# Kernel tuning notes

Hardware: AMD Instinct MI355X
Metric: run time of the kernel (lower is better)

## Reference

```python
import jax, jax.numpy as jnp
import numpy as np


def setup_inputs() -> dict:
    key = jax.random.key(0)
    ks = jax.random.split(key, 8)
    B, D, H1, H2, C = 262144, 256, 256, 128, 8
    s1 = 1.0 / np.sqrt(D)
    s2 = 1.0 / np.sqrt(H1)
    s3 = 1.0 / np.sqrt(H2)
    return {
        "x": jax.random.normal(ks[0], (B, D), dtype=jnp.float32),
        "W1": jax.random.normal(ks[1], (D, H1), dtype=jnp.float32) * s1,
        "b1": jnp.zeros((H1,), dtype=jnp.float32),
        "W2": jax.random.normal(ks[2], (H1, H2), dtype=jnp.float32) * s2,
        "b2": jnp.zeros((H2,), dtype=jnp.float32),
        "W3": jax.random.normal(ks[3], (H2, C), dtype=jnp.float32) * s3,
        "b3": jnp.zeros((C,), dtype=jnp.float32),
        "weibull_alpha": jnp.ones((C,), dtype=jnp.float32) * 2.0,
        "weibull_beta": jax.random.uniform(ks[4], (C,), dtype=jnp.float32, minval=0.5, maxval=2.0),
        "weibull_tau": jnp.zeros((C,), dtype=jnp.float32),
        "activation_vectors": jax.random.normal(ks[5], (C, H2), dtype=jnp.float32),
    }


def reference(x, W1, b1, W2, b2, W3, b3, weibull_alpha, weibull_beta, weibull_tau, activation_vectors):
    # MLP trunk (eval mode: dropout = identity)
    h = jax.nn.relu(x @ W1 + b1)          # [B, 256]
    act = jax.nn.relu(h @ W2 + b2)        # [B, H]
    logits = act @ W3 + b3                # [B, C]

    # per-class Euclidean distances via ||a-v||^2 = ||a||^2 - 2 a.v + ||v||^2
    a2 = jnp.sum(act * act, axis=1, keepdims=True)                 # [B, 1]
    v2 = jnp.sum(activation_vectors * activation_vectors, axis=1)  # [C]
    d2 = a2 - 2.0 * (act @ activation_vectors.T) + v2[None, :]     # [B, C]
    distances = jnp.sqrt(jnp.maximum(d2, 0.0))

    # Weibull CDF calibration, max over classes
    safe_beta = jnp.maximum(weibull_beta, 1e-6)                    # [C]
    safe_x = jnp.maximum(distances - weibull_tau[None, :], 0.0)    # [B, C]
    cdf = 1.0 - jnp.exp(-jnp.power(safe_x / safe_beta[None, :], weibull_alpha[None, :]))
    unknown_probs = jnp.max(cdf, axis=1)                           # [B]

    # conditional rescale of logits where unknown prob > 0.5
    scale = jnp.where(unknown_probs > 0.5, 1.0 - unknown_probs, 1.0)
    return logits * scale[:, None]
```

## Files before the change

kernel.cpp:

```cpp
#include <hip/hip_runtime.h>
#include <hip/hip_bf16.h>
#include <math.h>

typedef __attribute__((ext_vector_type(16))) float f32x16;

#define MFMA8(A, B, C) __builtin_amdgcn_mfma_f32_32x32x16_fp8_fp8((long)(A), (long)(B), (C), 0, 0, 0)

__device__ __forceinline__ int pk4(float a, float b, float c, float d) {
    int w = __builtin_amdgcn_cvt_pk_fp8_f32(a, b, 0, false);
    w = __builtin_amdgcn_cvt_pk_fp8_f32(c, d, w, true);
    return w;
}


__global__ void prep_pack(const float* __restrict__ W1, const float* __restrict__ W2,
                          const float* __restrict__ W3, const float* __restrict__ AV,
                          char* __restrict__ wp) {
    int j = blockIdx.x * 256 + threadIdx.x;
    float f[8];
    if (j < 8192) {
        int kc = j >> 8, m = j & 255;
        #pragma unroll
        for (int i = 0; i < 8; ++i) f[i] = W1[(kc * 8 + i) * 256 + m] * 16.f;
        int2 t; t.x = pk4(f[0], f[1], f[2], f[3]); t.y = pk4(f[4], f[5], f[6], f[7]);
        *(int2*)(wp + (size_t)j * 8) = t;
    } else if (j < 12288) {
        int jj = j - 8192; int kc = jj >> 7, m = jj & 127;
        #pragma unroll
        for (int i = 0; i < 8; ++i) f[i] = W2[(kc * 8 + i) * 128 + m] * 16.f;
        int2 t; t.x = pk4(f[0], f[1], f[2], f[3]); t.y = pk4(f[4], f[5], f[6], f[7]);
        *(int2*)(wp + 65536 + (size_t)jj * 8) = t;
    } else if (j < 12800) {
        int jj = j - 12288; int kc = jj >> 5, m = jj & 31;
        #pragma unroll
        for (int i = 0; i < 8; ++i) {
            int k = kc * 8 + i;
            float v = 0.f;
            if (m < 8)       v = W3[k * 8 + m] * 8.f;
            else if (m < 16) v = AV[(m - 8) * 128 + k];
            f[i] = v;
        }
        int2 t; t.x = pk4(f[0], f[1], f[2], f[3]); t.y = pk4(f[4], f[5], f[6], f[7]);
        *(int2*)(wp + 98304 + (size_t)jj * 8) = t;
    }
}

__global__ void prep_small(const float* __restrict__ AV, const float* __restrict__ b1,
                           const float* __restrict__ b2, float* __restrict__ v2,
                           float* __restrict__ b1p, float* __restrict__ b2p) {
    int t = threadIdx.x;
    {
        int mt = t >> 5, g = (t >> 4) & 1, r = t & 15;
        b1p[t] = b1[mt * 32 + 4 * g + (r & 3) + 8 * (r >> 2)];
    }
    if (t < 128) {
        int mt = t >> 5, g = (t >> 4) & 1, r = t & 15;
        b2p[t] = b2[mt * 32 + 4 * g + (r & 3) + 8 * (r >> 2)];
    }
    if (t < 64) {
        int c = t >> 3, jj = t & 7;
        float s = 0.f;
        for (int k = jj * 16; k < jj * 16 + 16; ++k) { float a = AV[c * 128 + k]; s = fmaf(a, a, s); }
        s += __shfl_xor(s, 1); s += __shfl_xor(s, 2); s += __shfl_xor(s, 4);
        if (jj == 0) v2[c] = s;
    }
}

#define LDS_H 16384

__global__ __launch_bounds__(256, 4)
void openmax_mfma(const float* __restrict__ x,
                  const float* __restrict__ b3,
                  const float* __restrict__ walpha, const float* __restrict__ wbeta,
                  const float* __restrict__ wtau,
                  const char* __restrict__ wpack, const float* __restrict__ v2g,
                  const float* __restrict__ b1p, const float* __restrict__ b2p,
                  float* __restrict__ out) {
    __shared__ __align__(16) char smem[32768];
    const int tid = threadIdx.x;
    const int l = tid & 63, wv = tid >> 6;
    const int lo = l & 31, g = l >> 5;
    const long row0 = (long)blockIdx.x * 64;

    const unsigned long long* Ap1 = (const unsigned long long*)wpack;
    const unsigned long long* Ap2 = (const unsigned long long*)(wpack + 65536);
    const unsigned long long* Ap3 = (const unsigned long long*)(wpack + 98304);

    const float4* xg = (const float4*)(x + row0 * 256);
    float4 xv[16];
    #pragma unroll
    for (int i = 0; i < 16; ++i) xv[i] = xg[i * 256 + tid];

    const int aRow1 = wv * 64 + lo;
    unsigned long long pa0[2], pa1[2];
    #pragma unroll
    for (int p = 0; p < 2; ++p) {
        int kc = p * 2 + g;
        pa0[p] = Ap1[kc * 256 + aRow1];
        pa1[p] = Ap1[kc * 256 + aRow1 + 32];
    }

    #pragma unroll
    for (int i = 0; i < 16; ++i) {
        int fc = i * 256 + tid;
        int row = fc >> 6, c4 = fc & 63;
        int hc = c4 >> 1, half = c4 & 1;
        int w = pk4(xv[i].x, xv[i].y, xv[i].z, xv[i].w);
        *(int*)(smem + row * 256 + (((hc ^ (row & 31)) << 3) + half * 4)) = w;
    }
    __syncthreads();

    {
        unsigned long long pb0[2], pb1[2];
        #pragma unroll
        for (int p = 0; p < 2; ++p) {
            int kc = p * 2 + g;
            pb0[p] = *(const unsigned long long*)(smem + lo * 256 + ((kc ^ lo) << 3));
            pb1[p] = *(const unsigned long long*)(smem + (32 + lo) * 256 + ((kc ^ lo) << 3));
        }
        f32x16 a00, a01, a10, a11;
        #pragma unroll
        for (int i = 0; i < 16; ++i) { a00[i] = 0.f; a01[i] = 0.f; a10[i] = 0.f; a11[i] = 0.f; }
        #pragma unroll
        for (int ks = 0; ks < 16; ++ks) {
            const int slot = ks & 1;
            unsigned long long A0 = pa0[slot], A1 = pa1[slot], B0 = pb0[slot], B1 = pb1[slot];
            if (ks < 14) {
                int kc = (ks + 2) * 2 + g;
                pa0[slot] = Ap1[kc * 256 + aRow1];
                pa1[slot] = Ap1[kc * 256 + aRow1 + 32];
                pb0[slot] = *(const unsigned long long*)(smem + lo * 256 + ((kc ^ lo) << 3));
                pb1[slot] = *(const unsigned long long*)(smem + (32 + lo) * 256 + ((kc ^ lo) << 3));
            }
            a00 = MFMA8(A0, B0, a00);
            a01 = MFMA8(A0, B1, a01);
            a10 = MFMA8(A1, B0, a10);
            a11 = MFMA8(A1, B1, a11);
        }
        #pragma unroll
        for (int mt = 0; mt < 2; ++mt) {
            const float* bp = b1p + ((wv * 2 + mt) * 2 + g) * 16;
            float bia[16];
            *(float4*)(bia)      = *(const float4*)(bp);
            *(float4*)(bia + 4)  = *(const float4*)(bp + 4);
            *(float4*)(bia + 8)  = *(const float4*)(bp + 8);
            *(float4*)(bia + 12) = *(const float4*)(bp + 12);
            #pragma unroll
            for (int nt = 0; nt < 2; ++nt) {
                const f32x16& A = (mt == 0) ? (nt == 0 ? a00 : a01)
                                            : (nt == 0 ? a10 : a11);
                int b = nt * 32 + lo;
                int base = LDS_H + b * 256 + g * 4;
                #pragma unroll
                for (int q = 0; q < 4; ++q) {
                    float v0 = fmaxf(fmaf(A[4 * q + 0], 0.0625f, bia[4 * q + 0]), 0.f);
                    float v1 = fmaxf(fmaf(A[4 * q + 1], 0.0625f, bia[4 * q + 1]), 0.f);
                    float v2_ = fmaxf(fmaf(A[4 * q + 2], 0.0625f, bia[4 * q + 2]), 0.f);
                    float v3 = fmaxf(fmaf(A[4 * q + 3], 0.0625f, bia[4 * q + 3]), 0.f);
                    int hc = (wv * 2 + mt) * 4 + q;
                    *(int*)(smem + base + ((hc ^ (b & 31)) << 3)) = pk4(v0, v1, v2_, v3);
                }
            }
        }
    }

    const int aRow2 = wv * 32 + lo;
    unsigned long long pa2[2];
    #pragma unroll
    for (int p = 0; p < 2; ++p) {
        int kc = p * 2 + g;
        pa2[p] = Ap2[kc * 128 + aRow2];
    }
    __syncthreads();

    {
        unsigned long long pb0[2], pb1[2];
        #pragma unroll
        for (int p = 0; p < 2; ++p) {
            int kc = p * 2 + g;
            pb0[p] = *(const unsigned long long*)(smem + LDS_H + lo * 256 + ((kc ^ lo) << 3));
            pb1[p] = *(const unsigned long long*)(smem + LDS_H + (32 + lo) * 256 + ((kc ^ lo) << 3));
        }
        f32x16 c0, c1;
        #pragma unroll
        for (int i = 0; i < 16; ++i) { c0[i] = 0.f; c1[i] = 0.f; }
        #pragma unroll
        for (int ks = 0; ks < 16; ++ks) {
            const int slot = ks & 1;
            unsigned long long A = pa2[slot], B0 = pb0[slot], B1 = pb1[slot];
            if (ks < 14) {
                int kc = (ks + 2) * 2 + g;
                pa2[slot] = Ap2[kc * 128 + aRow2];
                pb0[slot] = *(const unsigned long long*)(smem + LDS_H + lo * 256 + ((kc ^ lo) << 3));
                pb1[slot] = *(const unsigned long long*)(smem + LDS_H + (32 + lo) * 256 + ((kc ^ lo) << 3));
            }
            c0 = MFMA8(A, B0, c0);
            c1 = MFMA8(A, B1, c1);
        }
        const float* bp = b2p + (wv * 2 + g) * 16;
        float bia[16];
        *(float4*)(bia)      = *(const float4*)(bp);
        *(float4*)(bia + 4)  = *(const float4*)(bp + 4);
        *(float4*)(bia + 8)  = *(const float4*)(bp + 8);
        *(float4*)(bia + 12) = *(const float4*)(bp + 12);
        #pragma unroll
        for (int nt = 0; nt < 2; ++nt) {
            const f32x16& A = (nt == 0) ? c0 : c1;
            int b = nt * 32 + lo;
            int base = b * 128 + g * 4;
            float ss = 0.f;
            #pragma unroll
            for (int q = 0; q < 4; ++q) {
                float v0 = fmaxf(fmaf(A[4 * q + 0], 0.0625f, bia[4 * q + 0]), 0.f);
                float v1 = fmaxf(fmaf(A[4 * q + 1], 0.0625f, bia[4 * q + 1]), 0.f);
                float v2_ = fmaxf(fmaf(A[4 * q + 2], 0.0625f, bia[4 * q + 2]), 0.f);
                float v3 = fmaxf(fmaf(A[4 * q + 3], 0.0625f, bia[4 * q + 3]), 0.f);
                ss += v0 * v0 + v1 * v1 + v2_ * v2_ + v3 * v3;
                int ac = wv * 4 + q;
                *(int*)(smem + base + ((ac ^ (b & 15)) << 3)) = pk4(v0, v1, v2_, v3);
            }
            ss += __shfl_xor(ss, 32);
            if (g == 0) *(float*)(smem + 8192 + (wv * 64 + b) * 4) = ss;
        }
    }

    unsigned long long pa3[8];
    float4 e_b3[2], e_v2[2], e_al[2], e_be[2], e_ta[2];
    if (wv < 2) {
        #pragma unroll
        for (int p = 0; p < 8; ++p) {
            int kc = p * 2 + g;
            pa3[p] = Ap3[kc * 32 + lo];
        }
        e_b3[0] = *(const float4*)(b3);     e_b3[1] = *(const float4*)(b3 + 4);
        e_v2[0] = *(const float4*)(v2g);    e_v2[1] = *(const float4*)(v2g + 4);
        e_al[0] = *(const float4*)(walpha); e_al[1] = *(const float4*)(walpha + 4);
        e_be[0] = *(const float4*)(wbeta);  e_be[1] = *(const float4*)(wbeta + 4);
        e_ta[0] = *(const float4*)(wtau);   e_ta[1] = *(const float4*)(wtau + 4);
    }
    __syncthreads();

    if (wv < 2) {
        const int b = wv * 32 + lo;
        unsigned long long pb[8];
        #pragma unroll
        for (int p = 0; p < 8; ++p) {
            int kc = p * 2 + g;
            pb[p] = *(const unsigned long long*)(smem + b * 128 + ((kc ^ (b & 15)) << 3));
        }
        f32x16 acc;
        #pragma unroll
        for (int i = 0; i < 16; ++i) acc[i] = 0.f;
        #pragma unroll
        for (int ks = 0; ks < 8; ++ks)
            acc = MFMA8(pa3[ks], pb[ks], acc);

        float oth[8];
        #pragma unroll
        for (int j = 0; j < 8; ++j) oth[j] = __shfl_xor(acc[j], 32);

        float a2v = 0.f;
        #pragma unroll
        for (int wq = 0; wq < 4; ++wq)
            a2v += *(const float*)(smem + 8192 + (wq * 64 + b) * 4);

        float m = 0.f, outv[8];
        #pragma unroll
        for (int c = 0; c < 8; ++c) {
            float lgv = ((c >> 2) == g) ? acc[c & 3]       : oth[c & 3];
            float dtv = ((c >> 2) == g) ? acc[4 + (c & 3)] : oth[4 + (c & 3)];
            float v2c = e_v2[c >> 2][c & 3];
            float d2 = a2v - 2.f * dtv + v2c;
            float dist = sqrtf(fmaxf(d2, 0.f));
            float sb = fmaxf(e_be[c >> 2][c & 3], 1e-6f);
            float sx = fmaxf(dist - e_ta[c >> 2][c & 3], 0.f);
            float t = sx / sb;
            float y = exp2f(e_al[c >> 2][c & 3] * log2f(t));
            float cdf = 1.f - expf(-y);
            m = fmaxf(m, cdf);
            outv[c] = fmaf(lgv, 0.125f, e_b3[c >> 2][c & 3]);
        }
        float scale = (m > 0.5f) ? (1.f - m) : 1.f;
        if (g == 0) {
            float4 o0 = { outv[0] * scale, outv[1] * scale, outv[2] * scale, outv[3] * scale };
            float4 o1 = { outv[4] * scale, outv[5] * scale, outv[6] * scale, outv[7] * scale };
            float4* op = (float4*)(out + (row0 + b) * 8);
            op[0] = o0; op[1] = o1;
        }
    }
}

extern "C" void kernel_launch(void* const* d_in, const int* in_sizes, int n_in,
                              void* d_out, int out_size, void* d_ws, size_t ws_size,
                              hipStream_t stream) {
    const float* x      = (const float*)d_in[0];
    const float* W1     = (const float*)d_in[1];
    const float* b1     = (const float*)d_in[2];
    const float* W2     = (const float*)d_in[3];
    const float* b2     = (const float*)d_in[4];
    const float* W3     = (const float*)d_in[5];
    const float* b3     = (const float*)d_in[6];
    const float* walpha = (const float*)d_in[7];
    const float* wbeta  = (const float*)d_in[8];
    const float* wtau   = (const float*)d_in[9];
    const float* AV     = (const float*)d_in[10];
    float* out = (float*)d_out;

    char*  wpack = (char*)d_ws;
    float* v2    = (float*)((char*)d_ws + 102400);
    float* b1p   = (float*)((char*)d_ws + 102432);
    float* b2p   = (float*)((char*)d_ws + 103456);

    prep_pack<<<50, 256, 0, stream>>>(W1, W2, W3, AV, wpack);
    prep_small<<<1, 256, 0, stream>>>(AV, b1, b2, v2, b1p, b2p);

    const int B = in_sizes[0] / 256;
    openmax_mfma<<<B / 64, 256, 0, stream>>>(x, b3, walpha, wbeta, wtau,
                                             wpack, v2, b1p, b2p, out);
}
```

Before: 78.03 us.

## Merge prep kernels and split layer-1 MFMA by M-tile to raise occupancy

Folds the two small weight-prep kernels into one launch, using an extra block for the bias and norm work. Restructures the first-layer MFMA loop to run the two 32-row M-tiles one after another, cutting live accumulators from four to two, and raises launch bounds from 4 to 5 blocks per SM. The aim is lower register pressure for higher occupancy plus one less kernel launch. In exchange, the B operand is read from LDS twice and the MFMAs within each tile have fewer independent accumulators to interleave.

```diff
diff --git a/kernel.cpp b/kernel.cpp
--- a/kernel.cpp
+++ b/kernel.cpp
@@ -13,9 +13,31 @@
 }
 
 
-__global__ void prep_pack(const float* __restrict__ W1, const float* __restrict__ W2,
-                          const float* __restrict__ W3, const float* __restrict__ AV,
-                          char* __restrict__ wp) {
+__global__ void prep_all(const float* __restrict__ W1, const float* __restrict__ W2,
+                         const float* __restrict__ W3, const float* __restrict__ AV,
+                         const float* __restrict__ b1, const float* __restrict__ b2,
+                         char* __restrict__ wp,
+                         float* __restrict__ v2, float* __restrict__ b1p,
+                         float* __restrict__ b2p) {
+    if (blockIdx.x == 50) {
+        int t = threadIdx.x;
+        {
+            int mt = t >> 5, g = (t >> 4) & 1, r = t & 15;
+            b1p[t] = b1[mt * 32 + 4 * g + (r & 3) + 8 * (r >> 2)];
+        }
+        if (t < 128) {
+            int mt = t >> 5, g = (t >> 4) & 1, r = t & 15;
+            b2p[t] = b2[mt * 32 + 4 * g + (r & 3) + 8 * (r >> 2)];
+        }
+        if (t < 64) {
+            int c = t >> 3, jj = t & 7;
+            float s = 0.f;
+            for (int k = jj * 16; k < jj * 16 + 16; ++k) { float a = AV[c * 128 + k]; s = fmaf(a, a, s); }
+            s += __shfl_xor(s, 1); s += __shfl_xor(s, 2); s += __shfl_xor(s, 4);
+            if (jj == 0) v2[c] = s;
+        }
+        return;
+    }
     int j = blockIdx.x * 256 + threadIdx.x;
     float f[8];
     if (j < 8192) {
@@ -45,30 +67,9 @@
     }
 }
 
-__global__ void prep_small(const float* __restrict__ AV, const float* __restrict__ b1,
-                           const float* __restrict__ b2, float* __restrict__ v2,
-                           float* __restrict__ b1p, float* __restrict__ b2p) {
-    int t = threadIdx.x;
-    {
-        int mt = t >> 5, g = (t >> 4) & 1, r = t & 15;
-        b1p[t] = b1[mt * 32 + 4 * g + (r & 3) + 8 * (r >> 2)];
-    }
-    if (t < 128) {
-        int mt = t >> 5, g = (t >> 4) & 1, r = t & 15;
-        b2p[t] = b2[mt * 32 + 4 * g + (r & 3) + 8 * (r >> 2)];
-    }
-    if (t < 64) {
-        int c = t >> 3, jj = t & 7;
-        float s = 0.f;
-        for (int k = jj * 16; k < jj * 16 + 16; ++k) { float a = AV[c * 128 + k]; s = fmaf(a, a, s); }
-        s += __shfl_xor(s, 1); s += __shfl_xor(s, 2); s += __shfl_xor(s, 4);
-        if (jj == 0) v2[c] = s;
-    }
-}
-
 #define LDS_H 16384
 
-__global__ __launch_bounds__(256, 4)
+__global__ __launch_bounds__(256, 5)
 void openmax_mfma(const float* __restrict__ x,
                   const float* __restrict__ b3,
                   const float* __restrict__ walpha, const float* __restrict__ wbeta,
@@ -91,15 +92,6 @@
     #pragma unroll
     for (int i = 0; i < 16; ++i) xv[i] = xg[i * 256 + tid];
 
-    const int aRow1 = wv * 64 + lo;
-    unsigned long long pa0[2], pa1[2];
-    #pragma unroll
-    for (int p = 0; p < 2; ++p) {
-        int kc = p * 2 + g;
-        pa0[p] = Ap1[kc * 256 + aRow1];
-        pa1[p] = Ap1[kc * 256 + aRow1 + 32];
-    }
-
     #pragma unroll
     for (int i = 0; i < 16; ++i) {
         int fc = i * 256 + tid;
@@ -110,56 +102,52 @@
     }
     __syncthreads();
 
-    {
-        unsigned long long pb0[2], pb1[2];
+    #pragma unroll
+    for (int mt = 0; mt < 2; ++mt) {
+        const int aRow = (wv * 2 + mt) * 32 + lo;
+        unsigned long long pa[2], pb0[2], pb1[2];
         #pragma unroll
         for (int p = 0; p < 2; ++p) {
             int kc = p * 2 + g;
+            pa[p]  = Ap1[kc * 256 + aRow];
             pb0[p] = *(const unsigned long long*)(smem + lo * 256 + ((kc ^ lo) << 3));
             pb1[p] = *(const unsigned long long*)(smem + (32 + lo) * 256 + ((kc ^ lo) << 3));
         }
-        f32x16 a00, a01, a10, a11;
-        #pragma unroll
-        for (int i = 0; i < 16; ++i) { a00[i] = 0.f; a01[i] = 0.f; a10[i] = 0.f; a11[i] = 0.f; }
+        f32x16 a0, a1;
+        #pragma unroll
+        for (int i = 0; i < 16; ++i) { a0[i] = 0.f; a1[i] = 0.f; }
         #pragma unroll
         for (int ks = 0; ks < 16; ++ks) {
             const int slot = ks & 1;
-            unsigned long long A0 = pa0[slot], A1 = pa1[slot], B0 = pb0[slot], B1 = pb1[slot];
+            unsigned long long A = pa[slot], B0 = pb0[slot], B1 = pb1[slot];
             if (ks < 14) {
                 int kc = (ks + 2) * 2 + g;
-                pa0[slot] = Ap1[kc * 256 + aRow1];
-                pa1[slot] = Ap1[kc * 256 + aRow1 + 32];
+                pa[slot]  = Ap1[kc * 256 + aRow];
                 pb0[slot] = *(const unsigned long long*)(smem + lo * 256 + ((kc ^ lo) << 3));
                 pb1[slot] = *(const unsigned long long*)(smem + (32 + lo) * 256 + ((kc ^ lo) << 3));
             }
-            a00 = MFMA8(A0, B0, a00);
-            a01 = MFMA8(A0, B1, a01);
-            a10 = MFMA8(A1, B0, a10);
-            a11 = MFMA8(A1, B1, a11);
-        }
-        #pragma unroll
-        for (int mt = 0; mt < 2; ++mt) {
-            const float* bp = b1p + ((wv * 2 + mt) * 2 + g) * 16;
-            float bia[16];
-            *(float4*)(bia)      = *(const float4*)(bp);
-            *(float4*)(bia + 4)  = *(const float4*)(bp + 4);
-            *(float4*)(bia + 8)  = *(const float4*)(bp + 8);
-            *(float4*)(bia + 12) = *(const float4*)(bp + 12);
+            a0 = MFMA8(A, B0, a0);
+            a1 = MFMA8(A, B1, a1);
+        }
+        const float* bp = b1p + ((wv * 2 + mt) * 2 + g) * 16;
+        float bia[16];
+        *(float4*)(bia)      = *(const float4*)(bp);
+        *(float4*)(bia + 4)  = *(const float4*)(bp + 4);
+        *(float4*)(bia + 8)  = *(const float4*)(bp + 8);
+        *(float4*)(bia + 12) = *(const float4*)(bp + 12);
+        #pragma unroll
+        for (int nt = 0; nt < 2; ++nt) {
+            const f32x16& A = (nt == 0) ? a0 : a1;
+            int b = nt * 32 + lo;
+            int base = LDS_H + b * 256 + g * 4;
             #pragma unroll
-            for (int nt = 0; nt < 2; ++nt) {
-                const f32x16& A = (mt == 0) ? (nt == 0 ? a00 : a01)
-                                            : (nt == 0 ? a10 : a11);
-                int b = nt * 32 + lo;
-                int base = LDS_H + b * 256 + g * 4;
-                #pragma unroll
-                for (int q = 0; q < 4; ++q) {
-                    float v0 = fmaxf(fmaf(A[4 * q + 0], 0.0625f, bia[4 * q + 0]), 0.f);
-                    float v1 = fmaxf(fmaf(A[4 * q + 1], 0.0625f, bia[4 * q + 1]), 0.f);
-                    float v2_ = fmaxf(fmaf(A[4 * q + 2], 0.0625f, bia[4 * q + 2]), 0.f);
-                    float v3 = fmaxf(fmaf(A[4 * q + 3], 0.0625f, bia[4 * q + 3]), 0.f);
-                    int hc = (wv * 2 + mt) * 4 + q;
-                    *(int*)(smem + base + ((hc ^ (b & 31)) << 3)) = pk4(v0, v1, v2_, v3);
-                }
+            for (int q = 0; q < 4; ++q) {
+                float v0 = fmaxf(fmaf(A[4 * q + 0], 0.0625f, bia[4 * q + 0]), 0.f);
+                float v1 = fmaxf(fmaf(A[4 * q + 1], 0.0625f, bia[4 * q + 1]), 0.f);
+                float v2_ = fmaxf(fmaf(A[4 * q + 2], 0.0625f, bia[4 * q + 2]), 0.f);
+                float v3 = fmaxf(fmaf(A[4 * q + 3], 0.0625f, bia[4 * q + 3]), 0.f);
+                int hc = (wv * 2 + mt) * 4 + q;
+                *(int*)(smem + base + ((hc ^ (b & 31)) << 3)) = pk4(v0, v1, v2_, v3);
             }
         }
     }
@@ -311,8 +299,7 @@
     float* b1p   = (float*)((char*)d_ws + 102432);
     float* b2p   = (float*)((char*)d_ws + 103456);
 
-    prep_pack<<<50, 256, 0, stream>>>(W1, W2, W3, AV, wpack);
-    prep_small<<<1, 256, 0, stream>>>(AV, b1, b2, v2, b1p, b2p);
+    prep_all<<<51, 256, 0, stream>>>(W1, W2, W3, AV, b1, b2, wpack, v2, b1p, b2p);
 
     const int B = in_sizes[0] / 256;
     openmax_mfma<<<B / 64, 256, 0, stream>>>(x, b3, walpha, wbeta, wtau,
```

Result: slower. 113.9 us (+45.9%).
